# Kernel optimization log

Measured on AMD Instinct MI355X. Metric: run time of the kernel, lower is better.

The kernel has to match this reference:

```python
import jax, jax.numpy as jnp
import numpy as np

B, N, G, K, ENC = 8, 8192, 512, 32, 512
EPS = 1e-5


def setup_inputs() -> dict:
    key = jax.random.key(0)
    ks = jax.random.split(key, 8)
    def rn(k, shape, scale):
        return jax.random.normal(k, shape, dtype=jnp.float32) * scale
    return {
        "xyz": jax.random.normal(ks[0], (B, N, 3), dtype=jnp.float32),
        "color": jax.random.uniform(ks[1], (B, N, 3), dtype=jnp.float32),
        # Encoder.first_conv: Conv1d(6,128,1) -> LN(128) -> ReLU -> Conv1d(128,256,1)
        "w1": rn(ks[2], (128, 6), 0.4),   "b1": jnp.zeros((128,), jnp.float32),
        "g1": jnp.ones((128,), jnp.float32), "be1": jnp.zeros((128,), jnp.float32),
        "w2": rn(ks[3], (256, 128), 0.08), "b2": jnp.zeros((256,), jnp.float32),
        # Encoder.second_conv: Conv1d(512,512,1) -> LN(512) -> ReLU -> Conv1d(512,ENC,1)
        "w3": rn(ks[4], (512, 512), 0.04), "b3": jnp.zeros((512,), jnp.float32),
        "g2": jnp.ones((512,), jnp.float32), "be2": jnp.zeros((512,), jnp.float32),
        "w4": rn(ks[5], (ENC, 512), 0.04), "b4": jnp.zeros((ENC,), jnp.float32),
    }


def _fps_idx(xyz, num_samples):
    # Iterative farthest-point sampling, deterministic start at index 0 (pytorch3d default).
    b, n, _ = xyz.shape
    def body(carry, _):
        min_d, last = carry                                   # [B,N], [B]
        lp = jnp.take_along_axis(xyz, last[:, None, None], axis=1)  # [B,1,3]
        d = jnp.sum((xyz - lp) ** 2, axis=-1)                 # [B,N]
        min_d = jnp.minimum(min_d, d)
        nxt = jnp.argmax(min_d, axis=1).astype(jnp.int32)
        return (min_d, nxt), nxt
    init = (jnp.full((b, n), jnp.inf, dtype=xyz.dtype), jnp.zeros((b,), jnp.int32))
    _, rest = jax.lax.scan(body, init, None, length=num_samples - 1)
    return jnp.concatenate([jnp.zeros((1, b), jnp.int32), rest], axis=0).T  # [B,G]


def _layer_norm(x, g, b):
    mu = jnp.mean(x, axis=-1, keepdims=True)
    var = jnp.mean((x - mu) ** 2, axis=-1, keepdims=True)
    return (x - mu) * jax.lax.rsqrt(var + EPS) * g + b


def reference(xyz, color, w1, b1, g1, be1, w2, b2, w3, b3, g2, be2, w4, b4):
    # ---- Group: FPS centers + full pairwise sqdist + KNN top-k + gathers ----
    fidx = _fps_idx(xyz, G)                                   # [B,G]
    center = jax.vmap(lambda p, i: p[i])(xyz, fidx)           # [B,G,3]
    # square_distance(center, xyz) -> [B,G,N]
    d = (-2.0 * jnp.einsum('bgc,bnc->bgn', center, xyz)
         + jnp.sum(center ** 2, axis=-1)[:, :, None]
         + jnp.sum(xyz ** 2, axis=-1)[:, None, :])
    _, knn = jax.lax.top_k(-d, K)                             # [B,G,K] smallest distances
    gather = jax.vmap(lambda p, i: p[i])
    nbr_xyz = gather(xyz, knn.reshape(B, -1)).reshape(B, G, K, 3)
    nbr_col = gather(color, knn.reshape(B, -1)).reshape(B, G, K, 3)
    feats = jnp.concatenate([nbr_xyz - center[:, :, None, :], nbr_col], axis=-1)  # [B,G,K,6]
    # ---- Encoder: 1x1 convs == per-point linears (layer_norm variant) ----
    x = feats.reshape(B * G, K, 6)
    h = jnp.einsum('pkc,dc->pkd', x, w1) + b1                 # [BG,K,128]
    h = jax.nn.relu(_layer_norm(h, g1, be1))
    h = jnp.einsum('pkc,dc->pkd', h, w2) + b2                 # [BG,K,256]
    hg = jnp.max(h, axis=1, keepdims=True)                    # [BG,1,256] global max-pool
    h = jnp.concatenate([jnp.broadcast_to(hg, h.shape), h], axis=-1)  # [BG,K,512]
    h = jnp.einsum('pkc,dc->pkd', h, w3) + b3                 # [BG,K,512]
    h = jax.nn.relu(_layer_norm(h, g2, be2))
    h = jnp.einsum('pkc,dc->pkd', h, w4) + b4                 # [BG,K,ENC]
    return jnp.max(h, axis=1).reshape(B, G, ENC)
```

## Files before the change

### kernel.cpp

```cpp
#include <hip/hip_runtime.h>
#include <hip/hip_bf16.h>
#include <stdint.h>

constexpr int Bn = 8;
constexpr int Np = 8192;
constexpr int Gc = 512;
constexpr int Kn = 32;
constexpr int Mrows = Bn * Gc * Kn;
constexpr float LNEPS = 1e-5f;

using f32x2  = __attribute__((ext_vector_type(2))) float;
using f32x4  = __attribute__((ext_vector_type(4))) float;
using bf16x8 = __attribute__((ext_vector_type(8))) __bf16;

#define DEVINL __device__ __forceinline__

DEVINL unsigned wave_red_max_u32(unsigned x) {
    int v = (int)x, t;
    t = __builtin_amdgcn_update_dpp(0, v, 0x111, 0xf, 0xf, false); v = ((unsigned)v > (unsigned)t) ? v : t;
    t = __builtin_amdgcn_update_dpp(0, v, 0x112, 0xf, 0xf, false); v = ((unsigned)v > (unsigned)t) ? v : t;
    t = __builtin_amdgcn_update_dpp(0, v, 0x114, 0xf, 0xf, false); v = ((unsigned)v > (unsigned)t) ? v : t;
    t = __builtin_amdgcn_update_dpp(0, v, 0x118, 0xf, 0xf, false); v = ((unsigned)v > (unsigned)t) ? v : t;
    t = __builtin_amdgcn_update_dpp(0, v, 0x142, 0xa, 0xf, false); v = ((unsigned)v > (unsigned)t) ? v : t;
    t = __builtin_amdgcn_update_dpp(0, v, 0x143, 0xc, 0xf, false); v = ((unsigned)v > (unsigned)t) ? v : t;
    return (unsigned)__builtin_amdgcn_readlane(v, 63);
}
DEVINL unsigned wave_red_min_u32(unsigned x) {
    int v = (int)x, t;
    t = __builtin_amdgcn_update_dpp(-1, v, 0x111, 0xf, 0xf, false); v = ((unsigned)v < (unsigned)t) ? v : t;
    t = __builtin_amdgcn_update_dpp(-1, v, 0x112, 0xf, 0xf, false); v = ((unsigned)v < (unsigned)t) ? v : t;
    t = __builtin_amdgcn_update_dpp(-1, v, 0x114, 0xf, 0xf, false); v = ((unsigned)v < (unsigned)t) ? v : t;
    t = __builtin_amdgcn_update_dpp(-1, v, 0x118, 0xf, 0xf, false); v = ((unsigned)v < (unsigned)t) ? v : t;
    t = __builtin_amdgcn_update_dpp(-1, v, 0x142, 0xa, 0xf, false); v = ((unsigned)v < (unsigned)t) ? v : t;
    t = __builtin_amdgcn_update_dpp(-1, v, 0x143, 0xc, 0xf, false); v = ((unsigned)v < (unsigned)t) ? v : t;
    return (unsigned)__builtin_amdgcn_readlane(v, 63);
}
DEVINL unsigned long long wave_red_min_u64(unsigned long long x) {
    unsigned lo = (unsigned)x, hi = (unsigned)(x >> 32);
#define RSTEP(ctl, rm) { \
    unsigned tlo = (unsigned)__builtin_amdgcn_update_dpp(-1, (int)lo, ctl, rm, 0xf, false); \
    unsigned thi = (unsigned)__builtin_amdgcn_update_dpp(-1, (int)hi, ctl, rm, 0xf, false); \
    unsigned long long o = ((unsigned long long)thi << 32) | tlo; \
    unsigned long long c = ((unsigned long long)hi << 32) | lo; \
    if (o < c) { lo = tlo; hi = thi; } }
    RSTEP(0x111, 0xf) RSTEP(0x112, 0xf) RSTEP(0x114, 0xf) RSTEP(0x118, 0xf)
    RSTEP(0x142, 0xa) RSTEP(0x143, 0xc)
#undef RSTEP
    unsigned flo = (unsigned)__builtin_amdgcn_readlane((int)lo, 63);
    unsigned fhi = (unsigned)__builtin_amdgcn_readlane((int)hi, 63);
    return ((unsigned long long)fhi << 32) | flo;
}
DEVINL unsigned fkey(float f) {
    unsigned b = __float_as_uint(f);
    return b ^ (unsigned)(((int)b >> 31) | (int)0x80000000);
}

__global__ __launch_bounds__(512) void fps_kernel(const float* __restrict__ xyz,
                                                  float* __restrict__ centers)
{
    const int b = blockIdx.x;
    const int t = threadIdx.x;
    __shared__ f32x4 pts[Np];
    __shared__ unsigned long long sred[3];
    const float* P = xyz + (size_t)b * Np * 3;
    f32x2 X[8], Y[8], Z[8], MD[8];
#pragma unroll
    for (int i = 0; i < 8; ++i) {
        int p0 = (2 * i) * 512 + t;
        int p1 = p0 + 512;
        float x0 = P[p0 * 3 + 0], y0 = P[p0 * 3 + 1], z0 = P[p0 * 3 + 2];
        float x1 = P[p1 * 3 + 0], y1 = P[p1 * 3 + 1], z1 = P[p1 * 3 + 2];
        X[i] = f32x2{x0, x1}; Y[i] = f32x2{y0, y1}; Z[i] = f32x2{z0, z1};
        pts[p0] = f32x4{x0, y0, z0, 0.f};
        pts[p1] = f32x4{x1, y1, z1, 0.f};
        MD[i] = f32x2{__builtin_inff(), __builtin_inff()};
    }
    if (t < 3) sred[t] = 0ull;
    if (t == 0) {
        centers[(size_t)(b * Gc) * 3 + 0] = P[0];
        centers[(size_t)(b * Gc) * 3 + 1] = P[1];
        centers[(size_t)(b * Gc) * 3 + 2] = P[2];
    }
    __syncthreads();
    int last = 0;
    for (int g = 1; g < Gc; ++g) {
        const f32x4 c4 = pts[last];
        const f32x2 cx = {c4.x, c4.x}, cy = {c4.y, c4.y}, cz = {c4.z, c4.z};
        f32x2 bv2 = {0.f, 0.f};
#pragma unroll
        for (int i = 0; i < 8; ++i) {
            f32x2 dx = X[i] - cx;
            f32x2 dy = Y[i] - cy;
            f32x2 dz = Z[i] - cz;
            f32x2 d  = (dx * dx + dy * dy) + dz * dz;
            f32x2 m  = MD[i];
            m.x = fminf(m.x, d.x); m.y = fminf(m.y, d.y);
            MD[i] = m;
            bv2.x = fmaxf(bv2.x, m.x); bv2.y = fmaxf(bv2.y, m.y);
        }
        const float bv = fmaxf(bv2.x, bv2.y);
        const unsigned wmax = wave_red_max_u32(__float_as_uint(bv));
        unsigned idx = 0xffffffffu;
#pragma unroll
        for (int i = 7; i >= 0; --i) {
            if (__float_as_uint(MD[i].y) == wmax) idx = (unsigned)((2 * i + 1) * 512 + t);
            if (__float_as_uint(MD[i].x) == wmax) idx = (unsigned)((2 * i) * 512 + t);
        }
        const unsigned widx = wave_red_min_u32(idx);
        if ((t & 63) == 0) {
            unsigned long long pack =
                ((unsigned long long)wmax << 32) | (unsigned long long)(~widx);
            atomicMax(&sred[g % 3], pack);
        }
        if (t == 1) sred[(g + 1) % 3] = 0ull;
        __syncthreads();
        const unsigned long long w = sred[g % 3];
        const int wi = (int)(~(unsigned)w);
        if (t == 0) {
            f32x4 c = pts[wi];
            centers[(size_t)(b * Gc + g) * 3 + 0] = c.x;
            centers[(size_t)(b * Gc + g) * 3 + 1] = c.y;
            centers[(size_t)(b * Gc + g) * 3 + 2] = c.z;
        }
        last = wi;
    }
}

__global__ __launch_bounds__(256) void knn_feats_kernel(const float* __restrict__ xyz,
                                                        const float* __restrict__ color,
                                                        const float* __restrict__ centers,
                                                        float* __restrict__ feats)
{
    const int bg = blockIdx.x;
    const int b  = bg >> 9;
    const int t  = threadIdx.x;
    const int wave = t >> 6, lane = t & 63;
    __shared__ unsigned long long wl[128];
    const float cx = centers[(size_t)bg * 3 + 0];
    const float cy = centers[(size_t)bg * 3 + 1];
    const float cz = centers[(size_t)bg * 3 + 2];
    const float cc = __fadd_rn(__fadd_rn(__fmul_rn(cx, cx), __fmul_rn(cy, cy)), __fmul_rn(cz, cz));
    const float* P = xyz + (size_t)b * Np * 3;
    const int pbase = wave * 2048 + lane;
    float dr[32];
#pragma unroll
    for (int i = 0; i < 32; ++i) {
        int p = pbase + i * 64;
        float px = P[p * 3 + 0], py = P[p * 3 + 1], pz = P[p * 3 + 2];
        float dot = __fadd_rn(__fadd_rn(__fmul_rn(cx, px), __fmul_rn(cy, py)), __fmul_rn(cz, pz));
        float pp  = __fadd_rn(__fadd_rn(__fmul_rn(px, px), __fmul_rn(py, py)), __fmul_rn(pz, pz));
        dr[i] = __fadd_rn(__fadd_rn(__fmul_rn(-2.0f, dot), cc), pp);
    }
    unsigned excl = 0;
    for (int k = 0; k < Kn; ++k) {
        float bd = __builtin_inff();
        int   bs = 0;
#pragma unroll
        for (int i = 0; i < 32; ++i) {
            float d = ((excl >> i) & 1u) ? __builtin_inff() : dr[i];
            if (d < bd) { bd = d; bs = i; }
        }
        unsigned gidx = (unsigned)(pbase + bs * 64);
        unsigned long long win = wave_red_min_u64(
            ((unsigned long long)fkey(bd) << 32) | (unsigned long long)gidx);
        if (lane == 0) wl[wave * 32 + k] = win;
        unsigned widx = (unsigned)win;
        if ((widx & 63) == (unsigned)lane) excl |= 1u << ((widx >> 6) & 31);
    }
    __syncthreads();
    if (t < 128) {
        const unsigned long long my = wl[t];
        int rank = 0;
        for (int j = 0; j < 128; ++j) rank += (wl[j] < my) ? 1 : 0;
        if (rank < Kn) {
            unsigned gi = (unsigned)my;
            float px = P[gi * 3 + 0], py = P[gi * 3 + 1], pz = P[gi * 3 + 2];
            const float* C = color + (size_t)b * Np * 3;
            float* F = feats + (size_t)(bg * Kn + rank) * 6;
            F[0] = px - cx; F[1] = py - cy; F[2] = pz - cz;
            F[3] = C[gi * 3 + 0]; F[4] = C[gi * 3 + 1]; F[5] = C[gi * 3 + 2];
        }
    }
}

__global__ void cast_w_kernel(const float* __restrict__ w2, const float* __restrict__ w3,
                              const float* __restrict__ w4,
                              __hip_bfloat16* __restrict__ o2, __hip_bfloat16* __restrict__ o3,
                              __hip_bfloat16* __restrict__ o4)
{
    int i = blockIdx.x * 256 + threadIdx.x;
    if (i < 256 * 128) o2[i] = __float2bfloat16(w2[i]);
    o3[i] = __float2bfloat16(w3[i]);
    o4[i] = __float2bfloat16(w4[i]);
}

__global__ __launch_bounds__(256) void h1_kernel(const float* __restrict__ feats,
                                                 const float* __restrict__ w1,
                                                 const float* __restrict__ b1,
                                                 const float* __restrict__ g1,
                                                 const float* __restrict__ be1,
                                                 __hip_bfloat16* __restrict__ h1)
{
    const int gtid = blockIdx.x * 256 + threadIdx.x;
    const int row  = gtid >> 6;
    const int lane = gtid & 63;
    const float* f = feats + (size_t)row * 6;
    float fr[6];
#pragma unroll
    for (int i = 0; i < 6; ++i) fr[i] = f[i];
    const int c0 = lane * 2;
    float a0 = b1[c0], a1 = b1[c0 + 1];
#pragma unroll
    for (int i = 0; i < 6; ++i) {
        a0 = fmaf(w1[c0 * 6 + i], fr[i], a0);
        a1 = fmaf(w1[(c0 + 1) * 6 + i], fr[i], a1);
    }
    float s = a0 + a1;
#pragma unroll
    for (int m = 1; m < 64; m <<= 1) s += __shfl_xor(s, m, 64);
    float mu = s * (1.f / 128.f);
    float d0 = a0 - mu, d1 = a1 - mu;
    float q = d0 * d0 + d1 * d1;
#pragma unroll
    for (int m = 1; m < 64; m <<= 1) q += __shfl_xor(q, m, 64);
    float iv = rsqrtf(q * (1.f / 128.f) + LNEPS);
    float y0 = fmaxf(0.f, d0 * iv * g1[c0] + be1[c0]);
    float y1 = fmaxf(0.f, d1 * iv * g1[c0 + 1] + be1[c0 + 1]);
    __hip_bfloat16* dst = h1 + (size_t)row * 128 + c0;
    dst[0] = __float2bfloat16(y0);
    dst[1] = __float2bfloat16(y1);
}

template <int BN, int BK, int EPI>
__global__ __launch_bounds__(512, 2) void gemm_kernel(
    const __hip_bfloat16* A, int lda,
    const __hip_bfloat16* __restrict__ Bw, int ldb, int nkt,
    const float* __restrict__ bias,
    const float* __restrict__ gamma, const float* __restrict__ beta,
    __hip_bfloat16* outB, int ocol0,
    float* __restrict__ outF)
{
    constexpr int BM = 128;
    constexpr int WN = BN / 4;
    constexpr int NI = WN / 16;
    constexpr int MI = 4;
    constexpr int RB = BK * 2;
    constexpr int SWM = BK / 8 - 1;
    constexpr int A_ELE = BM * BK;
    constexpr int B_ELE = BN * BK;
    constexpr int BUF = A_ELE + B_ELE;
    constexpr int ACH = A_ELE * 2 / 16 / 512;
    constexpr int BCH = B_ELE * 2 / 16 / 512;
    __shared__ __hip_bfloat16 smem[2 * BUF];

    const int tid  = threadIdx.x;
    const int wid  = tid >> 6, lane = tid & 63;
    const int wm   = wid >> 2, wn = wid & 3;
    const int lrow = lane & 15, lq = lane >> 4;
    const int m0   = blockIdx.x * BM;

    f32x4 acc[MI][NI] = {};

    auto stage = [&](int buf, int k0) {
        const char* Ab = (const char*)A + ((size_t)m0 * lda + k0) * 2;
        const char* Bb = (const char*)Bw + (size_t)k0 * 2;
        char* sA = (char*)(smem + (size_t)buf * BUF);
        char* sB = sA + A_ELE * 2;
#pragma unroll
        for (int i = 0; i < ACH; ++i) {
            int chunk = i * 512 + tid;
            int Pp = chunk * 16;
            int row = Pp / RB;
            int kb = (Pp % RB) ^ ((row & SWM) << 4);
            const void* g = Ab + (size_t)row * (lda * 2) + kb;
            void* l = sA + (i * 512 + wid * 64) * 16;
            __builtin_amdgcn_global_load_lds((const __attribute__((address_space(1))) void*)g,
                                             (__attribute__((address_space(3))) void*)l, 16, 0, 0);
        }
#pragma unroll
        for (int i = 0; i < BCH; ++i) {
            int chunk = i * 512 + tid;
            int Pp = chunk * 16;
            int n = Pp / RB;
            int kb = (Pp % RB) ^ ((n & SWM) << 4);
            const void* g = Bb + (size_t)n * (ldb * 2) + kb;
            void* l = sB + (i * 512 + wid * 64) * 16;
            __builtin_amdgcn_global_load_lds((const __attribute__((address_space(1))) void*)g,
                                             (__attribute__((address_space(3))) void*)l, 16, 0, 0);
        }
    };

    auto compute = [&](int buf) {
        const char* sA = (const char*)(smem + (size_t)buf * BUF);
        const char* sB = sA + A_ELE * 2;
#pragma unroll
        for (int kk = 0; kk < BK / 32; ++kk) {
            bf16x8 af[MI], bfv[NI];
#pragma unroll
            for (int mi = 0; mi < MI; ++mi) {
                int row = wm * 64 + mi * 16 + lrow;
                int off = row * RB + ((kk * 64 + lq * 16) ^ ((row & SWM) << 4));
                af[mi] = *(const bf16x8*)(sA + off);
            }
#pragma unroll
            for (int ni = 0; ni < NI; ++ni) {
                int n = wn * WN + ni * 16 + lrow;
                int off = n * RB + ((kk * 64 + lq * 16) ^ ((n & SWM) << 4));
                bfv[ni] = *(const bf16x8*)(sB + off);
            }
#pragma unroll
            for (int mi = 0; mi < MI; ++mi)
#pragma unroll
                for (int ni = 0; ni < NI; ++ni)
                    acc[mi][ni] = __builtin_amdgcn_mfma_f32_16x16x32_bf16(af[mi], bfv[ni], acc[mi][ni], 0, 0, 0);
        }
    };

    stage(0, 0);
    __syncthreads();
    int cur = 0;
    for (int kt = 0; kt < nkt; ++kt) {
        if (kt + 1 < nkt) stage(cur ^ 1, (kt + 1) * BK);
        compute(cur);
        __syncthreads();
        cur ^= 1;
    }

    float bv[NI] = {};
    if constexpr (EPI != 6) {
#pragma unroll
        for (int ni = 0; ni < NI; ++ni) bv[ni] = bias[wn * WN + ni * 16 + lrow];
    }

    if constexpr (EPI == 3) {
#pragma unroll
        for (int mi = 0; mi < MI; ++mi)
#pragma unroll
            for (int ni = 0; ni < NI; ++ni) {
                int col = ocol0 + wn * WN + ni * 16 + lrow;
#pragma unroll
                for (int j = 0; j < 4; ++j) {
                    int row = wm * 64 + mi * 16 + lq * 4 + j;
                    outB[(size_t)(m0 + row) * 512 + col] = __float2bfloat16(acc[mi][ni][j] + bv[ni]);
                }
            }
        float* hgp = (float*)smem;
#pragma unroll
        for (int mi2 = 0; mi2 < 2; ++mi2) {
#pragma unroll
            for (int ni = 0; ni < NI; ++ni) {
                float m = -__builtin_inff();
#pragma unroll
                for (int mh = 0; mh < 2; ++mh) {
                    int mi = mi2 * 2 + mh;
#pragma unroll
                    for (int j = 0; j < 4; ++j) m = fmaxf(m, acc[mi][ni][j] + bv[ni]);
                }
                m = fmaxf(m, __shfl_xor(m, 16, 64));
                m = fmaxf(m, __shfl_xor(m, 32, 64));
                if (lq == 0)
                    hgp[(wm * 2 + mi2) * 256 + wn * WN + ni * 16 + lrow] = m;
            }
        }
        __syncthreads();
#pragma unroll 4
        for (int i = 0; i < 64; ++i) {
            int idx = i * 512 + tid;
            int row = idx >> 8, col = idx & 255;
            outB[(size_t)(m0 + row) * 512 + col] = __float2bfloat16(hgp[(row >> 5) * 256 + col]);
        }
    } else if constexpr (EPI == 4) {
#pragma unroll
        for (int mi = 0; mi < MI; ++mi)
#pragma unroll
            for (int ni = 0; ni < NI; ++ni) {
                int col = wn * WN + ni * 16 + lrow;
#pragma unroll
                for (int j = 0; j < 4; ++j) {
                    int row = wm * 64 + mi * 16 + lq * 4 + j;
                    outF[(size_t)(m0 + row) * 512 + col] = acc[mi][ni][j] + bv[ni];
                }
            }
    } else if constexpr (EPI == 1 || EPI == 6) {
        float gv[NI], bev[NI];
#pragma unroll
        for (int ni = 0; ni < NI; ++ni) {
            int col = wn * WN + ni * 16 + lrow;
            gv[ni] = gamma[col]; bev[ni] = beta[col];
        }
        if constexpr (EPI == 1) {
#pragma unroll
            for (int mi = 0; mi < MI; ++mi)
#pragma unroll
                for (int ni = 0; ni < NI; ++ni)
#pragma unroll
                    for (int j = 0; j < 4; ++j) acc[mi][ni][j] += bv[ni];
        } else {
            const float* P1 = outF;
#pragma unroll
            for (int mi = 0; mi < MI; ++mi) {
                int grow = (m0 >> 5) + wm * 2 + (mi >> 1);
#pragma unroll
                for (int ni = 0; ni < NI; ++ni) {
                    float ad = P1[(size_t)grow * 512 + (wn * WN + ni * 16 + lrow)];
#pragma unroll
                    for (int j = 0; j < 4; ++j) acc[mi][ni][j] += ad;
                }
            }
        }

        float* rs  = (float*)smem;
        float* rq  = rs + BM * 4;
        float* rmu = rq + BM * 4;
        float* riv = rmu + BM;
#pragma unroll
        for (int mi = 0; mi < MI; ++mi) {
#pragma unroll
            for (int j = 0; j < 4; ++j) {
                float s = 0.f, q = 0.f;
#pragma unroll
                for (int ni = 0; ni < NI; ++ni) { float v = acc[mi][ni][j]; s += v; q += v * v; }
#pragma unroll
                for (int m = 1; m < 16; m <<= 1) { s += __shfl_xor(s, m, 64); q += __shfl_xor(q, m, 64); }
                if (lrow == 0) {
                    int row = wm * 64 + mi * 16 + lq * 4 + j;
                    rs[row * 4 + wn] = s;
                    rq[row * 4 + wn] = q;
                }
            }
        }
        __syncthreads();
        if (tid < BM) {
            float S = rs[tid * 4 + 0] + rs[tid * 4 + 1] + rs[tid * 4 + 2] + rs[tid * 4 + 3];
            float Q = rq[tid * 4 + 0] + rq[tid * 4 + 1] + rq[tid * 4 + 2] + rq[tid * 4 + 3];
            float mu = S * (1.f / BN);
            float var = Q * (1.f / BN) - mu * mu;
            rmu[tid] = mu;
            riv[tid] = rsqrtf(var + LNEPS);
        }
        __syncthreads();
#pragma unroll
        for (int mi = 0; mi < MI; ++mi)
#pragma unroll
            for (int j = 0; j < 4; ++j) {
                int row = wm * 64 + mi * 16 + lq * 4 + j;
                float mu = rmu[row], iv = riv[row];
#pragma unroll
                for (int ni = 0; ni < NI; ++ni) {
                    float v = (acc[mi][ni][j] - mu) * iv * gv[ni] + bev[ni];
                    v = fmaxf(v, 0.f);
                    outB[(size_t)(m0 + row) * 512 + (wn * WN + ni * 16 + lrow)] = __float2bfloat16(v);
                }
            }
    } else {
#pragma unroll
        for (int grp = 0; grp < 2; ++grp) {
            float mx[NI];
#pragma unroll
            for (int ni = 0; ni < NI; ++ni) {
                float m = -__builtin_inff();
#pragma unroll
                for (int mh = 0; mh < 2; ++mh) {
                    int mi = grp * 2 + mh;
#pragma unroll
                    for (int j = 0; j < 4; ++j) m = fmaxf(m, acc[mi][ni][j] + bv[ni]);
                }
                mx[ni] = m;
            }
#pragma unroll
            for (int ni = 0; ni < NI; ++ni) {
                mx[ni] = fmaxf(mx[ni], __shfl_xor(mx[ni], 16, 64));
                mx[ni] = fmaxf(mx[ni], __shfl_xor(mx[ni], 32, 64));
            }
            if (lq == 0) {
                int grow = (m0 >> 5) + wm * 2 + grp;
#pragma unroll
                for (int ni = 0; ni < NI; ++ni)
                    outF[(size_t)grow * 512 + wn * WN + ni * 16 + lrow] = mx[ni];
            }
        }
    }
}

extern "C" void kernel_launch(void* const* d_in, const int* in_sizes, int n_in,
                              void* d_out, int out_size, void* d_ws, size_t ws_size,
                              hipStream_t stream)
{
    const float* xyz   = (const float*)d_in[0];
    const float* color = (const float*)d_in[1];
    const float* w1  = (const float*)d_in[2];
    const float* b1  = (const float*)d_in[3];
    const float* g1  = (const float*)d_in[4];
    const float* be1 = (const float*)d_in[5];
    const float* w2  = (const float*)d_in[6];
    const float* b2  = (const float*)d_in[7];
    const float* w3  = (const float*)d_in[8];
    const float* b3  = (const float*)d_in[9];
    const float* g2  = (const float*)d_in[10];
    const float* be2 = (const float*)d_in[11];
    const float* w4  = (const float*)d_in[12];
    const float* b4  = (const float*)d_in[13];
    float* out = (float*)d_out;

    char* ws = (char*)d_ws;
    size_t off = 0;
    auto alloc = [&](size_t bytes) -> void* {
        void* p = ws + off;
        off += (bytes + 255) & ~(size_t)255;
        return p;
    };
    float* centers      = (float*)alloc((size_t)Bn * Gc * 3 * 4);
    float* feats        = (float*)alloc((size_t)Mrows * 6 * 4);
    __hip_bfloat16* w2b = (__hip_bfloat16*)alloc((size_t)256 * 128 * 2);
    __hip_bfloat16* w3b = (__hip_bfloat16*)alloc((size_t)512 * 512 * 2);
    __hip_bfloat16* w4b = (__hip_bfloat16*)alloc((size_t)512 * 512 * 2);
    __hip_bfloat16* h1b = (__hip_bfloat16*)alloc((size_t)Mrows * 128 * 2);
    __hip_bfloat16* x3  = (__hip_bfloat16*)alloc((size_t)Mrows * 512 * 2);
    float* P1 = (float*)h1b;
    (void)ws_size; (void)in_sizes; (void)n_in; (void)out_size;

    fps_kernel<<<Bn, 512, 0, stream>>>(xyz, centers);
    knn_feats_kernel<<<Bn * Gc, 256, 0, stream>>>(xyz, color, centers, feats);
    cast_w_kernel<<<1024, 256, 0, stream>>>(w2, w3, w4, w2b, w3b, w4b);
    h1_kernel<<<Mrows / 4, 256, 0, stream>>>(feats, w1, b1, g1, be1, h1b);
    gemm_kernel<256, 32, 3><<<Mrows / 128, 512, 0, stream>>>(h1b, 128, w2b, 128, 4,  b2, nullptr, nullptr, x3, 256, nullptr);
    gemm_kernel<512, 32, 4><<<Bn * Gc / 128, 512, 0, stream>>>(x3, 512 * 32, w3b, 512, 8, b3, nullptr, nullptr, nullptr, 0, P1);
    gemm_kernel<512, 32, 6><<<Mrows / 128, 512, 0, stream>>>(x3 + 256, 512, w3b + 256, 512, 8, nullptr, g2, be2, x3, 0, P1);
    gemm_kernel<512, 32, 2><<<Mrows / 128, 512, 0, stream>>>(x3, 512, w4b, 512, 16, b4, nullptr, nullptr, nullptr, 0, out);
}
```

Measured before the change: 798.3 us.

## Fuse FPS, KNN and first layer into one persistent kernel with producer-consumer flags

Merges the FPS, KNN/feature-gather and h1 LayerNorm kernels into one launch of 256 blocks. Eight blocks run FPS and publish each center index via global atomic counters. The other 248 blocks spin-wait on those counters, then run KNN and the first linear+LN+ReLU for two centers at a time, writing bf16 h1 directly. This overlaps the serial FPS with neighbour search and removes the feats/centers round-trips and two launches. It relies on all 256 blocks being co-resident to avoid deadlock, and consumer blocks spend time spinning.

Result: slower. 1.095 ms (+37.2%).

```diff
diff --git a/kernel.cpp b/kernel.cpp
--- a/kernel.cpp
+++ b/kernel.cpp
@@ -55,131 +55,178 @@
     return b ^ (unsigned)(((int)b >> 31) | (int)0x80000000);
 }
 
-__global__ __launch_bounds__(512) void fps_kernel(const float* __restrict__ xyz,
-                                                  float* __restrict__ centers)
+__global__ __launch_bounds__(512) void fps_knn_h1_kernel(
+    const float* __restrict__ xyz, const float* __restrict__ color,
+    const float* __restrict__ w1, const float* __restrict__ b1,
+    const float* __restrict__ g1, const float* __restrict__ be1,
+    __hip_bfloat16* __restrict__ h1b,
+    unsigned* __restrict__ cnt, unsigned* __restrict__ cidx)
 {
-    const int b = blockIdx.x;
+    alignas(16) __shared__ char shraw[131104];
     const int t = threadIdx.x;
-    __shared__ f32x4 pts[Np];
-    __shared__ unsigned long long sred[3];
-    const float* P = xyz + (size_t)b * Np * 3;
-    f32x2 X[8], Y[8], Z[8], MD[8];
-#pragma unroll
-    for (int i = 0; i < 8; ++i) {
-        int p0 = (2 * i) * 512 + t;
-        int p1 = p0 + 512;
-        float x0 = P[p0 * 3 + 0], y0 = P[p0 * 3 + 1], z0 = P[p0 * 3 + 2];
-        float x1 = P[p1 * 3 + 0], y1 = P[p1 * 3 + 1], z1 = P[p1 * 3 + 2];
-        X[i] = f32x2{x0, x1}; Y[i] = f32x2{y0, y1}; Z[i] = f32x2{z0, z1};
-        pts[p0] = f32x4{x0, y0, z0, 0.f};
-        pts[p1] = f32x4{x1, y1, z1, 0.f};
-        MD[i] = f32x2{__builtin_inff(), __builtin_inff()};
+
+    if (blockIdx.x < 8) {
+        const int b = blockIdx.x;
+        f32x4* pts = (f32x4*)shraw;
+        unsigned long long* sred = (unsigned long long*)(shraw + 131072);
+        const float* P = xyz + (size_t)b * Np * 3;
+        f32x2 X[8], Y[8], Z[8], MD[8];
+#pragma unroll
+        for (int i = 0; i < 8; ++i) {
+            int p0 = (2 * i) * 512 + t;
+            int p1 = p0 + 512;
+            float x0 = P[p0 * 3 + 0], y0 = P[p0 * 3 + 1], z0 = P[p0 * 3 + 2];
+            float x1 = P[p1 * 3 + 0], y1 = P[p1 * 3 + 1], z1 = P[p1 * 3 + 2];
+            X[i] = f32x2{x0, x1}; Y[i] = f32x2{y0, y1}; Z[i] = f32x2{z0, z1};
+            pts[p0] = f32x4{x0, y0, z0, 0.f};
+            pts[p1] = f32x4{x1, y1, z1, 0.f};
+            MD[i] = f32x2{__builtin_inff(), __builtin_inff()};
+        }
+        if (t < 3) sred[t] = 0ull;
+        if (t == 0) {
+            __hip_atomic_store(&cidx[b * Gc + 0], 0u, __ATOMIC_RELAXED, __HIP_MEMORY_SCOPE_AGENT);
+            __hip_atomic_fetch_add(&cnt[b], 1u, __ATOMIC_RELEASE, __HIP_MEMORY_SCOPE_AGENT);
+        }
+        __syncthreads();
+        int last = 0;
+        for (int g = 1; g < Gc; ++g) {
+            const f32x4 c4 = pts[last];
+            const f32x2 cx = {c4.x, c4.x}, cy = {c4.y, c4.y}, cz = {c4.z, c4.z};
+            f32x2 bv2 = {0.f, 0.f};
+#pragma unroll
+            for (int i = 0; i < 8; ++i) {
+                f32x2 dx = X[i] - cx;
+                f32x2 dy = Y[i] - cy;
+                f32x2 dz = Z[i] - cz;
+                f32x2 d  = (dx * dx + dy * dy) + dz * dz;
+                f32x2 m  = MD[i];
+                m.x = fminf(m.x, d.x); m.y = fminf(m.y, d.y);
+                MD[i] = m;
+                bv2.x = fmaxf(bv2.x, m.x); bv2.y = fmaxf(bv2.y, m.y);
+            }
+            const float bv = fmaxf(bv2.x, bv2.y);
+            const unsigned wmax = wave_red_max_u32(__float_as_uint(bv));
+            unsigned idx = 0xffffffffu;
+#pragma unroll
+            for (int i = 7; i >= 0; --i) {
+                if (__float_as_uint(MD[i].y) == wmax) idx = (unsigned)((2 * i + 1) * 512 + t);
+                if (__float_as_uint(MD[i].x) == wmax) idx = (unsigned)((2 * i) * 512 + t);
+            }
+            const unsigned widx = wave_red_min_u32(idx);
+            if ((t & 63) == 0) {
+                unsigned long long pack =
+                    ((unsigned long long)wmax << 32) | (unsigned long long)(~widx);
+                atomicMax(&sred[g % 3], pack);
+            }
+            if (t == 1) sred[(g + 1) % 3] = 0ull;
+            __syncthreads();
+            const unsigned long long w = sred[g % 3];
+            const int wi = (int)(~(unsigned)w);
+            if (t == 0) {
+                __hip_atomic_store(&cidx[b * Gc + g], (unsigned)wi, __ATOMIC_RELAXED, __HIP_MEMORY_SCOPE_AGENT);
+                __hip_atomic_fetch_add(&cnt[b], 1u, __ATOMIC_RELEASE, __HIP_MEMORY_SCOPE_AGENT);
+            }
+            last = wi;
+        }
+        return;
     }
-    if (t < 3) sred[t] = 0ull;
-    if (t == 0) {
-        centers[(size_t)(b * Gc) * 3 + 0] = P[0];
-        centers[(size_t)(b * Gc) * 3 + 1] = P[1];
-        centers[(size_t)(b * Gc) * 3 + 2] = P[2];
-    }
-    __syncthreads();
-    int last = 0;
-    for (int g = 1; g < Gc; ++g) {
-        const f32x4 c4 = pts[last];
-        const f32x2 cx = {c4.x, c4.x}, cy = {c4.y, c4.y}, cz = {c4.z, c4.z};
-        f32x2 bv2 = {0.f, 0.f};
-#pragma unroll
-        for (int i = 0; i < 8; ++i) {
-            f32x2 dx = X[i] - cx;
-            f32x2 dy = Y[i] - cy;
-            f32x2 dz = Z[i] - cz;
-            f32x2 d  = (dx * dx + dy * dy) + dz * dz;
-            f32x2 m  = MD[i];
-            m.x = fminf(m.x, d.x); m.y = fminf(m.y, d.y);
-            MD[i] = m;
-            bv2.x = fmaxf(bv2.x, m.x); bv2.y = fmaxf(bv2.y, m.y);
-        }
-        const float bv = fmaxf(bv2.x, bv2.y);
-        const unsigned wmax = wave_red_max_u32(__float_as_uint(bv));
-        unsigned idx = 0xffffffffu;
-#pragma unroll
-        for (int i = 7; i >= 0; --i) {
-            if (__float_as_uint(MD[i].y) == wmax) idx = (unsigned)((2 * i + 1) * 512 + t);
-            if (__float_as_uint(MD[i].x) == wmax) idx = (unsigned)((2 * i) * 512 + t);
-        }
-        const unsigned widx = wave_red_min_u32(idx);
-        if ((t & 63) == 0) {
-            unsigned long long pack =
-                ((unsigned long long)wmax << 32) | (unsigned long long)(~widx);
-            atomicMax(&sred[g % 3], pack);
-        }
-        if (t == 1) sred[(g + 1) % 3] = 0ull;
-        __syncthreads();
-        const unsigned long long w = sred[g % 3];
-        const int wi = (int)(~(unsigned)w);
+
+    const int cid  = blockIdx.x - 8;
+    const int cb   = cid & 7;
+    const int cj   = cid >> 3;
+    const int wave = t >> 6;
+    const int sub  = wave & 3;
+    const int gsel = wave >> 2;
+    const int lane = t & 63;
+    unsigned long long* wl = (unsigned long long*)shraw;
+    float* fs = (float*)(shraw + 2048);
+    const float* P = xyz + (size_t)cb * Np * 3;
+    const float* C = color + (size_t)cb * Np * 3;
+    const int pbase = sub * 2048 + lane;
+
+    for (int p = cj; p < 256; p += 31) {
+        const int g = 2 * p + gsel;
         if (t == 0) {
-            f32x4 c = pts[wi];
-            centers[(size_t)(b * Gc + g) * 3 + 0] = c.x;
-            centers[(size_t)(b * Gc + g) * 3 + 1] = c.y;
-            centers[(size_t)(b * Gc + g) * 3 + 2] = c.z;
-        }
-        last = wi;
-    }
-}
-
-__global__ __launch_bounds__(256) void knn_feats_kernel(const float* __restrict__ xyz,
-                                                        const float* __restrict__ color,
-                                                        const float* __restrict__ centers,
-                                                        float* __restrict__ feats)
-{
-    const int bg = blockIdx.x;
-    const int b  = bg >> 9;
-    const int t  = threadIdx.x;
-    const int wave = t >> 6, lane = t & 63;
-    __shared__ unsigned long long wl[128];
-    const float cx = centers[(size_t)bg * 3 + 0];
-    const float cy = centers[(size_t)bg * 3 + 1];
-    const float cz = centers[(size_t)bg * 3 + 2];
-    const float cc = __fadd_rn(__fadd_rn(__fmul_rn(cx, cx), __fmul_rn(cy, cy)), __fmul_rn(cz, cz));
-    const float* P = xyz + (size_t)b * Np * 3;
-    const int pbase = wave * 2048 + lane;
-    float dr[32];
-#pragma unroll
-    for (int i = 0; i < 32; ++i) {
-        int p = pbase + i * 64;
-        float px = P[p * 3 + 0], py = P[p * 3 + 1], pz = P[p * 3 + 2];
-        float dot = __fadd_rn(__fadd_rn(__fmul_rn(cx, px), __fmul_rn(cy, py)), __fmul_rn(cz, pz));
-        float pp  = __fadd_rn(__fadd_rn(__fmul_rn(px, px), __fmul_rn(py, py)), __fmul_rn(pz, pz));
-        dr[i] = __fadd_rn(__fadd_rn(__fmul_rn(-2.0f, dot), cc), pp);
-    }
-    unsigned excl = 0;
-    for (int k = 0; k < Kn; ++k) {
-        float bd = __builtin_inff();
-        int   bs = 0;
+            while ((int)__hip_atomic_load(&cnt[cb], __ATOMIC_ACQUIRE, __HIP_MEMORY_SCOPE_AGENT) < 2 * p + 2)
+                __builtin_amdgcn_s_sleep(8);
+        }
+        __syncthreads();
+        const unsigned wic = __hip_atomic_load(&cidx[cb * Gc + g], __ATOMIC_RELAXED, __HIP_MEMORY_SCOPE_AGENT);
+        const float cx = P[wic * 3 + 0], cy = P[wic * 3 + 1], cz = P[wic * 3 + 2];
+        const float cc = __fadd_rn(__fadd_rn(__fmul_rn(cx, cx), __fmul_rn(cy, cy)), __fmul_rn(cz, cz));
+        float dr[32];
 #pragma unroll
         for (int i = 0; i < 32; ++i) {
-            float d = ((excl >> i) & 1u) ? __builtin_inff() : dr[i];
-            if (d < bd) { bd = d; bs = i; }
-        }
-        unsigned gidx = (unsigned)(pbase + bs * 64);
-        unsigned long long win = wave_red_min_u64(
-            ((unsigned long long)fkey(bd) << 32) | (unsigned long long)gidx);
-        if (lane == 0) wl[wave * 32 + k] = win;
-        unsigned widx = (unsigned)win;
-        if ((widx & 63) == (unsigned)lane) excl |= 1u << ((widx >> 6) & 31);
-    }
-    __syncthreads();
-    if (t < 128) {
-        const unsigned long long my = wl[t];
-        int rank = 0;
-        for (int j = 0; j < 128; ++j) rank += (wl[j] < my) ? 1 : 0;
-        if (rank < Kn) {
-            unsigned gi = (unsigned)my;
-            float px = P[gi * 3 + 0], py = P[gi * 3 + 1], pz = P[gi * 3 + 2];
-            const float* C = color + (size_t)b * Np * 3;
-            float* F = feats + (size_t)(bg * Kn + rank) * 6;
-            F[0] = px - cx; F[1] = py - cy; F[2] = pz - cz;
-            F[3] = C[gi * 3 + 0]; F[4] = C[gi * 3 + 1]; F[5] = C[gi * 3 + 2];
-        }
+            int pp = pbase + i * 64;
+            float px = P[pp * 3 + 0], py = P[pp * 3 + 1], pz = P[pp * 3 + 2];
+            float dot = __fadd_rn(__fadd_rn(__fmul_rn(cx, px), __fmul_rn(cy, py)), __fmul_rn(cz, pz));
+            float q   = __fadd_rn(__fadd_rn(__fmul_rn(px, px), __fmul_rn(py, py)), __fmul_rn(pz, pz));
+            dr[i] = __fadd_rn(__fadd_rn(__fmul_rn(-2.0f, dot), cc), q);
+        }
+        unsigned excl = 0;
+        for (int k = 0; k < Kn; ++k) {
+            float bd = __builtin_inff();
+            int   bs = 0;
+#pragma unroll
+            for (int i = 0; i < 32; ++i) {
+                float d = ((excl >> i) & 1u) ? __builtin_inff() : dr[i];
+                if (d < bd) { bd = d; bs = i; }
+            }
+            unsigned gidx = (unsigned)(pbase + bs * 64);
+            unsigned long long win = wave_red_min_u64(
+                ((unsigned long long)fkey(bd) << 32) | (unsigned long long)gidx);
+            if (lane == 0) wl[gsel * 128 + sub * 32 + k] = win;
+            unsigned widx = (unsigned)win;
+            if ((widx & 63) == (unsigned)lane) excl |= 1u << ((widx >> 6) & 31);
+        }
+        __syncthreads();
+        {
+            const int tt = t & 255, half = t >> 8;
+            if (tt < 128) {
+                const unsigned long long my = wl[half * 128 + tt];
+                int rank = 0;
+                for (int j = 0; j < 128; ++j) rank += (wl[half * 128 + j] < my) ? 1 : 0;
+                if (rank < Kn) {
+                    unsigned gi = (unsigned)my;
+                    float px = P[gi * 3 + 0], py = P[gi * 3 + 1], pz = P[gi * 3 + 2];
+                    float* F = fs + (half * 32 + rank) * 6;
+                    F[0] = px - cx; F[1] = py - cy; F[2] = pz - cz;
+                    F[3] = C[gi * 3 + 0]; F[4] = C[gi * 3 + 1]; F[5] = C[gi * 3 + 2];
+                }
+            }
+        }
+        __syncthreads();
+#pragma unroll
+        for (int rr = 0; rr < 8; ++rr) {
+            const int r  = wave * 8 + rr;
+            const int gg = r >> 5, k = r & 31;
+            const float* F = fs + (gg * 32 + k) * 6;
+            float fr[6];
+#pragma unroll
+            for (int i = 0; i < 6; ++i) fr[i] = F[i];
+            const int c0 = lane * 2;
+            float a0 = b1[c0], a1 = b1[c0 + 1];
+#pragma unroll
+            for (int i = 0; i < 6; ++i) {
+                a0 = fmaf(w1[c0 * 6 + i], fr[i], a0);
+                a1 = fmaf(w1[(c0 + 1) * 6 + i], fr[i], a1);
+            }
+            float s = a0 + a1;
+#pragma unroll
+            for (int m = 1; m < 64; m <<= 1) s += __shfl_xor(s, m, 64);
+            float mu = s * (1.f / 128.f);
+            float d0 = a0 - mu, d1 = a1 - mu;
+            float q = d0 * d0 + d1 * d1;
+#pragma unroll
+            for (int m = 1; m < 64; m <<= 1) q += __shfl_xor(q, m, 64);
+            float iv = rsqrtf(q * (1.f / 128.f) + LNEPS);
+            float y0 = fmaxf(0.f, d0 * iv * g1[c0] + be1[c0]);
+            float y1 = fmaxf(0.f, d1 * iv * g1[c0 + 1] + be1[c0 + 1]);
+            __hip_bfloat16* dst = h1b + ((size_t)(cb * Gc + 2 * p + gg) * 32 + k) * 128 + c0;
+            dst[0] = __float2bfloat16(y0);
+            dst[1] = __float2bfloat16(y1);
+        }
+        __syncthreads();
     }
 }
 
@@ -192,43 +239,6 @@
     if (i < 256 * 128) o2[i] = __float2bfloat16(w2[i]);
     o3[i] = __float2bfloat16(w3[i]);
     o4[i] = __float2bfloat16(w4[i]);
-}
-
-__global__ __launch_bounds__(256) void h1_kernel(const float* __restrict__ feats,
-                                                 const float* __restrict__ w1,
-                                                 const float* __restrict__ b1,
-                                                 const float* __restrict__ g1,
-                                                 const float* __restrict__ be1,
-                                                 __hip_bfloat16* __restrict__ h1)
-{
-    const int gtid = blockIdx.x * 256 + threadIdx.x;
-    const int row  = gtid >> 6;
-    const int lane = gtid & 63;
-    const float* f = feats + (size_t)row * 6;
-    float fr[6];
-#pragma unroll
-    for (int i = 0; i < 6; ++i) fr[i] = f[i];
-    const int c0 = lane * 2;
-    float a0 = b1[c0], a1 = b1[c0 + 1];
-#pragma unroll
-    for (int i = 0; i < 6; ++i) {
-        a0 = fmaf(w1[c0 * 6 + i], fr[i], a0);
-        a1 = fmaf(w1[(c0 + 1) * 6 + i], fr[i], a1);
-    }
-    float s = a0 + a1;
-#pragma unroll
-    for (int m = 1; m < 64; m <<= 1) s += __shfl_xor(s, m, 64);
-    float mu = s * (1.f / 128.f);
-    float d0 = a0 - mu, d1 = a1 - mu;
-    float q = d0 * d0 + d1 * d1;
-#pragma unroll
-    for (int m = 1; m < 64; m <<= 1) q += __shfl_xor(q, m, 64);
-    float iv = rsqrtf(q * (1.f / 128.f) + LNEPS);
-    float y0 = fmaxf(0.f, d0 * iv * g1[c0] + be1[c0]);
-    float y1 = fmaxf(0.f, d1 * iv * g1[c0 + 1] + be1[c0 + 1]);
-    __hip_bfloat16* dst = h1 + (size_t)row * 128 + c0;
-    dst[0] = __float2bfloat16(y0);
-    dst[1] = __float2bfloat16(y1);
 }
 
 template <int BN, int BK, int EPI>
@@ -381,21 +391,14 @@
                     outF[(size_t)(m0 + row) * 512 + col] = acc[mi][ni][j] + bv[ni];
                 }
             }
-    } else if constexpr (EPI == 1 || EPI == 6) {
+    } else if constexpr (EPI == 6) {
         float gv[NI], bev[NI];
 #pragma unroll
         for (int ni = 0; ni < NI; ++ni) {
             int col = wn * WN + ni * 16 + lrow;
             gv[ni] = gamma[col]; bev[ni] = beta[col];
         }
-        if constexpr (EPI == 1) {
-#pragma unroll
-            for (int mi = 0; mi < MI; ++mi)
-#pragma unroll
-                for (int ni = 0; ni < NI; ++ni)
-#pragma unroll
-                    for (int j = 0; j < 4; ++j) acc[mi][ni][j] += bv[ni];
-        } else {
+        {
             const float* P1 = outF;
 #pragma unroll
             for (int mi = 0; mi < MI; ++mi) {
@@ -509,8 +512,8 @@
         off += (bytes + 255) & ~(size_t)255;
         return p;
     };
-    float* centers      = (float*)alloc((size_t)Bn * Gc * 3 * 4);
-    float* feats        = (float*)alloc((size_t)Mrows * 6 * 4);
+    unsigned* cnt       = (unsigned*)alloc(8 * 4);
+    unsigned* cidx      = (unsigned*)alloc((size_t)Bn * Gc * 4);
     __hip_bfloat16* w2b = (__hip_bfloat16*)alloc((size_t)256 * 128 * 2);
     __hip_bfloat16* w3b = (__hip_bfloat16*)alloc((size_t)512 * 512 * 2);
     __hip_bfloat16* w4b = (__hip_bfloat16*)alloc((size_t)512 * 512 * 2);
@@ -519,10 +522,9 @@
     float* P1 = (float*)h1b;
     (void)ws_size; (void)in_sizes; (void)n_in; (void)out_size;
 
-    fps_kernel<<<Bn, 512, 0, stream>>>(xyz, centers);
-    knn_feats_kernel<<<Bn * Gc, 256, 0, stream>>>(xyz, color, centers, feats);
+    hipMemsetAsync(cnt, 0, 8 * 4, stream);
+    fps_knn_h1_kernel<<<256, 512, 0, stream>>>(xyz, color, w1, b1, g1, be1, h1b, cnt, cidx);
     cast_w_kernel<<<1024, 256, 0, stream>>>(w2, w3, w4, w2b, w3b, w4b);
-    h1_kernel<<<Mrows / 4, 256, 0, stream>>>(feats, w1, b1, g1, be1, h1b);
     gemm_kernel<256, 32, 3><<<Mrows / 128, 512, 0, stream>>>(h1b, 128, w2b, 128, 4,  b2, nullptr, nullptr, x3, 256, nullptr);
     gemm_kernel<512, 32, 4><<<Bn * Gc / 128, 512, 0, stream>>>(x3, 512 * 32, w3b, 512, 8, b3, nullptr, nullptr, nullptr, 0, P1);
     gemm_kernel<512, 32, 6><<<Mrows / 128, 512, 0, stream>>>(x3 + 256, 512, w3b + 256, 512, 8, nullptr, g2, be2, x3, 0, P1);
```
